# Kernel optimization log

Hardware: AMD Instinct MI355X
Metric: run time of the kernel (lower is better)

Reference implementation:

```python
import jax, jax.numpy as jnp
import numpy as np

B, T, ICD, H = 64, 256, 2000, 384
L, CH, W = 3, H // 3, 10  # levels, chunk_size, conv window


def setup_inputs() -> dict:
    key = jax.random.key(0)
    ks = jax.random.split(key, 10)
    s = 0.05
    return {
        "x": jax.random.uniform(ks[0], (B, T, ICD), jnp.float32),
        "dia_w": jax.random.normal(ks[1], (ICD, H), jnp.float32) * s,
        "dia_b": jnp.zeros((H,), jnp.float32),
        "kernel_w": jax.random.normal(ks[2], (H + 1, 4 * H + 2 * L), jnp.float32) * s,
        "kernel_b": jnp.zeros((4 * H + 2 * L,), jnp.float32),
        "rec_w": jax.random.normal(ks[3], (H + 1, 4 * H + 2 * L), jnp.float32) * s,
        "rec_b": jnp.zeros((4 * H + 2 * L,), jnp.float32),
        "scale_w": jax.random.normal(ks[4], (H, H // 6), jnp.float32) * s,
        "scale_b": jnp.zeros((H // 6,), jnp.float32),
        "rescale_w": jax.random.normal(ks[5], (H // 6, H), jnp.float32) * s,
        "rescale_b": jnp.zeros((H,), jnp.float32),
        "conv_w": jax.random.normal(ks[6], (H, H, W), jnp.float32) * s,  # (out, in, k)
        "conv_b": jnp.zeros((H,), jnp.float32),
        "out_w": jax.random.normal(ks[7], (H, ICD), jnp.float32) * s,
        "out_b": jnp.zeros((ICD,), jnp.float32),
        "choice": 0,  # 0 == 'dia'
    }


def _cumax_l2r(x):
    return jnp.cumsum(jax.nn.softmax(x, -1), -1)


def _cumax_r2l(x):
    return jnp.flip(jnp.cumsum(jax.nn.softmax(jnp.flip(x, -1), -1), -1), -1)


def _forward(x, dia_w, dia_b, kernel_w, kernel_b, rec_w, rec_b,
             scale_w, scale_b, rescale_w, rescale_b, conv_w, conv_b,
             out_w, out_b):
    embed = x @ dia_w + dia_b  # (B,T,H), choice='dia'
    Bs = embed.shape[0]
    ones = jnp.ones((Bs, 1), embed.dtype)  # interval T == 1

    def step(carry, xt):
        c, h, tmp_h, tmp_dis = carry
        xo = (jnp.concatenate([xt, ones], -1) @ kernel_w + kernel_b
              + jnp.concatenate([h, ones], -1) @ rec_w + rec_b)
        fm = _cumax_l2r(xo[:, :L])[:, :, None]          # (B,L,1)
        im = _cumax_r2l(xo[:, L:2 * L])[:, :, None]     # (B,L,1)
        g = xo[:, 2 * L:].reshape(Bs, 4 * L, CH)
        f = jax.nn.sigmoid(g[:, :L])
        i = jax.nn.sigmoid(g[:, L:2 * L])
        o = jax.nn.sigmoid(g[:, 2 * L:3 * L])
        c_in = jnp.tanh(g[:, 3 * L:])
        c_last = c.reshape(Bs, L, CH)
        ov = fm * im
        c_new = ov * (f * c_last + i * c_in) + (fm - ov) * c_last + (im - ov) * c_in
        h_new = (o * jnp.tanh(c_new)).reshape(Bs, H)
        c_new = c_new.reshape(Bs, H)
        cur_dis = 1.0 - jnp.mean(fm[..., 0], -1)        # (B,)
        tmp_h = jnp.concatenate([tmp_h[1:], h_new[None]], 0)      # (W,B,H)
        tmp_dis = jnp.concatenate([tmp_dis[1:], cur_dis[None]], 0)  # (W,B)
        local_dis = jax.nn.softmax(jnp.cumsum(tmp_dis.T, 1), 1)   # (B,W)
        local_h = tmp_h.transpose(1, 2, 0) * local_dis[:, None, :]  # (B,H,W)
        theme = jax.nn.sigmoid(
            jax.nn.relu(jnp.mean(local_h, -1) @ scale_w + scale_b) @ rescale_w + rescale_b)
        conv = jnp.einsum('bhw,ohw->bo', local_h, conv_w) + conv_b  # Conv1d, full-width kernel
        return (c_new, h_new, tmp_h, tmp_dis), (h_new, theme * conv)

    carry0 = (jnp.zeros((Bs, H), embed.dtype), jnp.zeros((Bs, H), embed.dtype),
              jnp.zeros((W, Bs, H), embed.dtype), jnp.zeros((W, Bs), embed.dtype))
    _, (origin_h, loc_h) = jax.lax.scan(step, carry0, embed.transpose(1, 0, 2))
    rnn = (origin_h + loc_h).transpose(1, 0, 2)  # (B,T,H); dropout off (eval)
    return rnn @ out_w + out_b                   # (B,T,ICD)


def reference(x, dia_w, dia_b, kernel_w, kernel_b, rec_w, rec_b,
              scale_w, scale_b, rescale_w, rescale_b, conv_w, conv_b,
              out_w, out_b, choice):
    # choice==0 -> 'dia' embedding path
    return _forward(x, dia_w, dia_b, kernel_w, kernel_b, rec_w, rec_b,
                    scale_w, scale_b, rescale_w, rescale_b, conv_w, conv_b,
                    out_w, out_b)
```

## Files before the change

### kernel.cpp

```cpp
#include <hip/hip_runtime.h>
#include <hip/hip_bf16.h>
#include <cstdint>
#include <cstddef>

#define B_DIM   64
#define T_DIM   256
#define ICD_DIM 2000
#define H_DIM   384
#define CH_DIM  128
#define W_WIN   10
#define M_DIM   (B_DIM * T_DIM)
#define XO_DIM  1542
#define XO_PAD  1664
#define K_X     2016
#define KCONV   3840
#define N_OUTP  2048

typedef unsigned short ushort_t;
typedef unsigned int   uint_t;
typedef __attribute__((ext_vector_type(8))) short short8;
typedef __attribute__((ext_vector_type(4))) float f32x4;
typedef __attribute__((ext_vector_type(2))) _Float16 f16x2;

__device__ __forceinline__ ushort_t f2bf(float v) {
    __hip_bfloat16 b = __float2bfloat16(v);
    ushort_t u; __builtin_memcpy(&u, &b, 2); return u;
}
__device__ __forceinline__ float bf2f(ushort_t u) {
    __hip_bfloat16 b; __builtin_memcpy(&b, &u, 2); return __bfloat162float(b);
}
__device__ __forceinline__ float sigmoidf_(float x) { return 1.f / (1.f + expf(-x)); }
__device__ __forceinline__ f16x2 asf16x2(uint_t u) { f16x2 h; __builtin_memcpy(&h, &u, 4); return h; }
__device__ __forceinline__ uint_t pkf16(float a, float b) {
    f16x2 h; h.x = (_Float16)a; h.y = (_Float16)b;
    uint_t u; __builtin_memcpy(&u, &h, 4); return u;
}
__device__ __forceinline__ float dot2f(uint_t a, uint_t b, float acc) {
#if __has_builtin(__builtin_amdgcn_fdot2)
    return __builtin_amdgcn_fdot2(asf16x2(a), asf16x2(b), acc, false);
#else
    f16x2 ha = asf16x2(a), hb = asf16x2(b);
    return acc + (float)ha.x * (float)hb.x + (float)ha.y * (float)hb.y;
#endif
}

__global__ void prep_dia(const float* __restrict__ dia_w, ushort_t* __restrict__ hi, ushort_t* __restrict__ lo)
{
    int id = blockIdx.x * 256 + threadIdx.x;
    if (id >= H_DIM * K_X) return;
    int n = id / K_X, k = id - n * K_X;
    float v = (k < ICD_DIM) ? dia_w[(size_t)k * H_DIM + n] : 0.f;
    ushort_t h = f2bf(v);
    hi[id] = h; lo[id] = f2bf(v - bf2f(h));
}
__global__ void prep_ker(const float* __restrict__ kernel_w, ushort_t* __restrict__ hi, ushort_t* __restrict__ lo)
{
    int id = blockIdx.x * 256 + threadIdx.x;
    if (id >= XO_PAD * H_DIM) return;
    int n = id / H_DIM, k = id - n * H_DIM;
    float v = (n < XO_DIM) ? kernel_w[(size_t)k * XO_DIM + n] : 0.f;
    ushort_t h = f2bf(v);
    hi[id] = h; lo[id] = f2bf(v - bf2f(h));
}
__global__ void prep_conv(const float* __restrict__ conv_w, ushort_t* __restrict__ bt)
{
    int id = blockIdx.x * 256 + threadIdx.x;
    if (id >= H_DIM * KCONV) return;
    int o = id / KCONV, k = id - o * KCONV;
    int w = k / H_DIM, h = k - w * H_DIM;
    bt[id] = f2bf(conv_w[((size_t)o * H_DIM + h) * W_WIN + w]);
}
__global__ void prep_out(const float* __restrict__ out_w, ushort_t* __restrict__ bt)
{
    int id = blockIdx.x * 256 + threadIdx.x;
    if (id >= N_OUTP * H_DIM) return;
    int n = id / H_DIM, k = id - n * H_DIM;
    bt[id] = f2bf((n < ICD_DIM) ? out_w[(size_t)k * ICD_DIM + n] : 0.f);
}
__global__ void prep_misc(const float* __restrict__ kernel_w, const float* __restrict__ kernel_b,
                          const float* __restrict__ rec_w, const float* __restrict__ rec_b,
                          const float* __restrict__ out_b,
                          float* __restrict__ bias2p, float* __restrict__ outbp)
{
    int j = blockIdx.x * 256 + threadIdx.x;
    if (j < XO_PAD)
        bias2p[j] = (j < XO_DIM) ? (kernel_w[(size_t)H_DIM * XO_DIM + j] + kernel_b[j]
                                  + rec_w[(size_t)H_DIM * XO_DIM + j] + rec_b[j]) : 0.f;
    if (j < N_OUTP)
        outbp[j] = (j < ICD_DIM) ? out_b[j] : 0.f;
}
__global__ void prep_rec2(const float* __restrict__ rec_w, uint_t* __restrict__ recg, uint_t* __restrict__ recm)
{
    int id = blockIdx.x * 256 + threadIdx.x;
    const int NG = 4 * 2 * 96 * 384;
    if (id < NG) {
        int cg = id % 384;
        int kk = (id / 384) % 96;
        int half = (id / (384 * 96)) & 1;
        int q = id / (384 * 96 * 2);
        int p = half * 96 + kk;
        int j = 6 + (cg >> 5) * 128 + q * 32 + (cg & 31);
        recg[id] = pkf16(rec_w[(size_t)(2 * p) * XO_DIM + j], rec_w[(size_t)(2 * p + 1) * XO_DIM + j]);
    } else if (id < NG + 6 * 192) {
        int id2 = id - NG;
        int mc = id2 / 192, p = id2 % 192;
        recm[id2] = pkf16(rec_w[(size_t)(2 * p) * XO_DIM + mc], rec_w[(size_t)(2 * p + 1) * XO_DIM + mc]);
    }
}

template<int MODE>
__global__ __launch_bounds__(256)
void mfma_gemm(const float* __restrict__ Af,
               const ushort_t* __restrict__ Abh, const ushort_t* __restrict__ Abl,
               const ushort_t* __restrict__ Bh, const ushort_t* __restrict__ Bl,
               float* __restrict__ Cf, ushort_t* __restrict__ Cb,
               ushort_t* __restrict__ Ehi, ushort_t* __restrict__ Elo,
               const float* __restrict__ bias,
               const ushort_t* __restrict__ theme,
               const float* __restrict__ hall, const float* __restrict__ ldwp,
               int ksteps, int kdim)
{
    constexpr bool SPLIT = (MODE <= 1);
    __shared__ ushort_t AhS[4096];
    __shared__ ushort_t BhS[4096];
    __shared__ ushort_t AlS[4096];
    __shared__ ushort_t BlS[4096];

    const int tid = threadIdx.x;
    const int rc = tid & 127, kh = tid >> 7;
    const int m0 = blockIdx.y * 128, n0 = blockIdx.x * 128;
    const int kq0 = kh * 2;

    const int lane = tid & 63, wid = tid >> 6;
    const int wm = wid >> 1, wn = wid & 1;
    const int l15 = lane & 15, lkq = lane >> 4;

    f32x4 acc[4][4];
#pragma unroll
    for (int i = 0; i < 4; ++i)
#pragma unroll
        for (int j = 0; j < 4; ++j)
#pragma unroll
            for (int q = 0; q < 4; ++q) acc[i][j][q] = 0.f;

    for (int ks = 0; ks < ksteps; ++ks) {
        const int k16 = ks * 32 + kh * 16;
        __syncthreads();

        if constexpr (MODE == 0 || MODE == 2) {
            float v[16];
            bool ok;
            if constexpr (MODE == 0) {
                ok = (k16 < ICD_DIM);
                if (ok) {
                    const float* ap = Af + (size_t)(m0 + rc) * ICD_DIM + k16;
#pragma unroll
                    for (int q = 0; q < 4; ++q) {
                        float4 t = *(const float4*)(ap + q * 4);
                        v[q * 4 + 0] = t.x; v[q * 4 + 1] = t.y; v[q * 4 + 2] = t.z; v[q * 4 + 3] = t.w;
                    }
                }
            } else {
                const int w = k16 / H_DIM, h0i = k16 - (k16 / H_DIM) * H_DIM;
                const int gm = m0 + rc, b = gm >> 8, tt = gm & 255;
                const int tp = tt - (W_WIN - 1) + w;
                ok = (tp >= 0);
                if (ok) {
                    const float lw = ldwp[(size_t)gm * W_WIN + w];
                    const float* ap = hall + ((size_t)(b * T_DIM + tp)) * H_DIM + h0i;
#pragma unroll
                    for (int q = 0; q < 4; ++q) {
                        float4 t = *(const float4*)(ap + q * 4);
                        v[q * 4 + 0] = t.x * lw; v[q * 4 + 1] = t.y * lw;
                        v[q * 4 + 2] = t.z * lw; v[q * 4 + 3] = t.w * lw;
                    }
                }
            }
            if (!ok) {
#pragma unroll
                for (int q = 0; q < 16; ++q) v[q] = 0.f;
            }
            uint_t hh[8], ll[8];
#pragma unroll
            for (int i = 0; i < 8; ++i) {
                ushort_t h0 = f2bf(v[2 * i]), h1 = f2bf(v[2 * i + 1]);
                hh[i] = (uint_t)h0 | ((uint_t)h1 << 16);
                if constexpr (SPLIT) {
                    ushort_t l0 = f2bf(v[2 * i] - bf2f(h0)), l1 = f2bf(v[2 * i + 1] - bf2f(h1));
                    ll[i] = (uint_t)l0 | ((uint_t)l1 << 16);
                }
            }
            *(uint4*)&AhS[(kq0 * 128 + rc) * 8]       = make_uint4(hh[0], hh[1], hh[2], hh[3]);
            *(uint4*)&AhS[((kq0 + 1) * 128 + rc) * 8] = make_uint4(hh[4], hh[5], hh[6], hh[7]);
            if constexpr (SPLIT) {
                *(uint4*)&AlS[(kq0 * 128 + rc) * 8]       = make_uint4(ll[0], ll[1], ll[2], ll[3]);
                *(uint4*)&AlS[((kq0 + 1) * 128 + rc) * 8] = make_uint4(ll[4], ll[5], ll[6], ll[7]);
            }
        } else {
            const ushort_t* ap = ((MODE == 1) ? Ehi : Abh) + (size_t)(m0 + rc) * H_DIM + k16;
            *(uint4*)&AhS[(kq0 * 128 + rc) * 8]       = *(const uint4*)ap;
            *(uint4*)&AhS[((kq0 + 1) * 128 + rc) * 8] = *(const uint4*)(ap + 8);
            if constexpr (MODE == 1) {
                const ushort_t* ap2 = Elo + (size_t)(m0 + rc) * H_DIM + k16;
                *(uint4*)&AlS[(kq0 * 128 + rc) * 8]       = *(const uint4*)ap2;
                *(uint4*)&AlS[((kq0 + 1) * 128 + rc) * 8] = *(const uint4*)(ap2 + 8);
            }
        }

        {
            const ushort_t* bp = Bh + (size_t)(n0 + rc) * kdim + k16;
            *(uint4*)&BhS[(kq0 * 128 + rc) * 8]       = *(const uint4*)bp;
            *(uint4*)&BhS[((kq0 + 1) * 128 + rc) * 8] = *(const uint4*)(bp + 8);
            if constexpr (SPLIT) {
                const ushort_t* bp2 = Bl + (size_t)(n0 + rc) * kdim + k16;
                *(uint4*)&BlS[(kq0 * 128 + rc) * 8]       = *(const uint4*)bp2;
                *(uint4*)&BlS[((kq0 + 1) * 128 + rc) * 8] = *(const uint4*)(bp2 + 8);
            }
        }
        __syncthreads();

        short8 ah[4], bh[4], al[4], bl[4];
#pragma unroll
        for (int mf = 0; mf < 4; ++mf)
            ah[mf] = *(const short8*)&AhS[(lkq * 128 + wm * 64 + mf * 16 + l15) * 8];
#pragma unroll
        for (int nf = 0; nf < 4; ++nf)
            bh[nf] = *(const short8*)&BhS[(lkq * 128 + wn * 64 + nf * 16 + l15) * 8];
        if constexpr (SPLIT) {
#pragma unroll
            for (int mf = 0; mf < 4; ++mf)
                al[mf] = *(const short8*)&AlS[(lkq * 128 + wm * 64 + mf * 16 + l15) * 8];
#pragma unroll
            for (int nf = 0; nf < 4; ++nf)
                bl[nf] = *(const short8*)&BlS[(lkq * 128 + wn * 64 + nf * 16 + l15) * 8];
        }
#pragma unroll
        for (int mf = 0; mf < 4; ++mf)
#pragma unroll
            for (int nf = 0; nf < 4; ++nf) {
                acc[mf][nf] = __builtin_amdgcn_mfma_f32_16x16x32_bf16(ah[mf], bh[nf], acc[mf][nf], 0, 0, 0);
                if constexpr (SPLIT) {
                    acc[mf][nf] = __builtin_amdgcn_mfma_f32_16x16x32_bf16(ah[mf], bl[nf], acc[mf][nf], 0, 0, 0);
                    acc[mf][nf] = __builtin_amdgcn_mfma_f32_16x16x32_bf16(al[mf], bh[nf], acc[mf][nf], 0, 0, 0);
                }
            }
    }

#pragma unroll
    for (int mf = 0; mf < 4; ++mf)
#pragma unroll
        for (int nf = 0; nf < 4; ++nf)
#pragma unroll
            for (int j = 0; j < 4; ++j) {
                const int gm = m0 + wm * 64 + mf * 16 + lkq * 4 + j;
                const int gn = n0 + wn * 64 + nf * 16 + l15;
                float v = acc[mf][nf][j] + bias[gn];
                if constexpr (MODE == 0) {
                    ushort_t h = f2bf(v);
                    Ehi[(size_t)gm * H_DIM + gn] = h;
                    Elo[(size_t)gm * H_DIM + gn] = f2bf(v - bf2f(h));
                } else if constexpr (MODE == 1) {
                    if (gn < XO_DIM) Cf[(size_t)gm * XO_DIM + gn] = v;
                } else if constexpr (MODE == 2) {
                    const size_t ix = (size_t)gm * H_DIM + gn;
                    v = v * bf2f(theme[ix]) + hall[ix];
                    Cb[ix] = f2bf(v);
                } else {
                    if (gn < ICD_DIM) Cf[(size_t)gm * ICD_DIM + gn] = v;
                }
            }
}

__global__ __launch_bounds__(768, 3)
void scan_kernel(const float* __restrict__ Xproj, const uint_t* __restrict__ recg,
                 const uint_t* __restrict__ recm, float* __restrict__ h_all,
                 float* __restrict__ dis_all, uint_t* __restrict__ hpk)
{
    __shared__ ushort_t hs16[H_DIM];
    __shared__ float xo_s[384];
    __shared__ float xom_s[6];
    __shared__ uint_t wm2[6 * 192];
    __shared__ float c_s[96];
    __shared__ float fm_s[3], im_s[3];

    const int tid = threadIdx.x;
    const int q = blockIdx.x >> 6, b = blockIdx.x & 63;

    const int cg = tid >> 1, half = tid & 1;
    const int jg = 6 + (cg >> 5) * 128 + q * 32 + (cg & 31);

    const int gl = tid / 32, gu = tid & 31;
    const int jglob = gl * 128 + q * 32 + gu;

    for (int i = tid; i < 6 * 192; i += 768) wm2[i] = recm[i];
    if (tid < H_DIM) hs16[tid] = 0;
    if (tid < 96) c_s[tid] = 0.f;

    uint_t w[96];
#pragma unroll
    for (int kk = 0; kk < 96; ++kk)
        w[kk] = recg[(size_t)((q * 2 + half) * 96 + kk) * 384 + cg];

    float xv = 0.f, xvm = 0.f;
    if (half == 0) xv = Xproj[((size_t)b * T_DIM + 0) * XO_DIM + jg];
    if (tid < 24 && (tid & 3) == 0) xvm = Xproj[((size_t)b * T_DIM + 0) * XO_DIM + (tid >> 2)];

    __syncthreads();

    for (int t = 0; t < T_DIM; ++t) {
        {
            float acc = 0.f;
            const ushort_t* hp = &hs16[half * 192];
#pragma unroll
            for (int kk = 0; kk < 96; kk += 4) {
                const uint4 hq = *(const uint4*)(hp + kk * 2);
                acc = dot2f(w[kk + 0], hq.x, acc);
                acc = dot2f(w[kk + 1], hq.y, acc);
                acc = dot2f(w[kk + 2], hq.z, acc);
                acc = dot2f(w[kk + 3], hq.w, acc);
            }
            acc += __shfl_xor(acc, 1);
            if (half == 0) xo_s[cg] = acc + xv;
        }
        if (tid < 24) {
            const int mc = tid >> 2, kq = tid & 3;
            float acc = 0.f;
            const uint_t* wp = &wm2[mc * 192 + kq * 48];
#pragma unroll
            for (int kk = 0; kk < 48; kk += 4) {
                const uint4 hq = *(const uint4*)&hs16[(kq * 48 + kk) * 2];
                acc = dot2f(wp[kk + 0], hq.x, acc);
                acc = dot2f(wp[kk + 1], hq.y, acc);
                acc = dot2f(wp[kk + 2], hq.z, acc);
                acc = dot2f(wp[kk + 3], hq.w, acc);
            }
            acc += __shfl_xor(acc, 2);
            acc += __shfl_xor(acc, 1);
            if (kq == 0) xom_s[mc] = acc + xvm;
        }
        __syncthreads();

        if (tid == 0) {
            float x0 = xom_s[0], x1 = xom_s[1], x2 = xom_s[2];
            float mx = fmaxf(x0, fmaxf(x1, x2));
            float e0 = expf(x0 - mx), e1 = expf(x1 - mx), e2 = expf(x2 - mx);
            float inv = 1.f / (e0 + e1 + e2);
            const float f0 = e0 * inv, f1 = (e0 + e1) * inv;
            fm_s[0] = f0; fm_s[1] = f1; fm_s[2] = 1.f;
            x0 = xom_s[3]; x1 = xom_s[4]; x2 = xom_s[5];
            mx = fmaxf(x0, fmaxf(x1, x2));
            e0 = expf(x0 - mx); e1 = expf(x1 - mx); e2 = expf(x2 - mx);
            inv = 1.f / (e0 + e1 + e2);
            im_s[0] = 1.f; im_s[1] = (e1 + e2) * inv; im_s[2] = e2 * inv;
            if (q == 0)
                dis_all[b * T_DIM + t] = 1.f - (f0 + f1 + 1.f) * (1.f / 3.f);
        }
        __syncthreads();

        if (tid < 96) {
            const float fm = fm_s[gl], im = im_s[gl];
            const float fg = sigmoidf_(xo_s[gl * 32 + gu]);
            const float ig = sigmoidf_(xo_s[(3 + gl) * 32 + gu]);
            const float og = sigmoidf_(xo_s[(6 + gl) * 32 + gu]);
            const float ci = tanhf(xo_s[(9 + gl) * 32 + gu]);
            const float cl = c_s[tid];
            const float ov = fm * im;
            const float cn = ov * (fg * cl + ig * ci) + (fm - ov) * cl + (im - ov) * ci;
            c_s[tid] = cn;
            const float hn = og * tanhf(cn);
            h_all[((size_t)b * T_DIM + t) * H_DIM + jglob] = hn;
            _Float16 hf = (_Float16)hn;
            ushort_t hb; __builtin_memcpy(&hb, &hf, 2);
            const uint_t word = ((uint_t)hb << 16) | (uint_t)(t + 1);
            __hip_atomic_store(&hpk[(size_t)(t & 1) * B_DIM * H_DIM + b * H_DIM + jglob],
                               word, __ATOMIC_RELAXED, __HIP_MEMORY_SCOPE_AGENT);
        }

        if (t + 1 < T_DIM) {
            if (half == 0) xv = Xproj[((size_t)b * T_DIM + (t + 1)) * XO_DIM + jg];
            if (tid < 24 && (tid & 3) == 0) xvm = Xproj[((size_t)b * T_DIM + (t + 1)) * XO_DIM + (tid >> 2)];
        }

        if (t + 1 < T_DIM) {
            if (tid < H_DIM) {
                const uint_t want = (uint_t)(t + 1);
                uint_t* addr = &hpk[(size_t)(t & 1) * B_DIM * H_DIM + b * H_DIM + tid];
                uint_t v = __hip_atomic_load(addr, __ATOMIC_RELAXED, __HIP_MEMORY_SCOPE_AGENT);
                while ((v & 0xFFFFu) != want) {
                    __builtin_amdgcn_s_sleep(1);
                    v = __hip_atomic_load(addr, __ATOMIC_RELAXED, __HIP_MEMORY_SCOPE_AGENT);
                }
                hs16[tid] = (ushort_t)(v >> 16);
            }
            __syncthreads();
        }
    }
}

__global__ __launch_bounds__(256, 2)
void locdis2_kernel(const float* __restrict__ h_all, const float* __restrict__ dis_all,
                    const float* __restrict__ scale_w, const float* __restrict__ scale_b,
                    const float* __restrict__ rescale_w, const float* __restrict__ rescale_b,
                    float* __restrict__ ldw, ushort_t* __restrict__ theme)
{
    __shared__ float ld_all[64][10];
    __shared__ uint_t mh2[192];
    __shared__ float part_s[4][64];
    __shared__ float hid[64];
    __shared__ uint_t hid2[32];

    const int tid = threadIdx.x;
    const int b = blockIdx.x >> 2, t0 = (blockIdx.x & 3) * 64;

    const int o1 = tid & 63, p1 = tid >> 6;
    uint_t w1[48];
#pragma unroll
    for (int kk = 0; kk < 48; ++kk) {
        const int p = p1 * 48 + kk;
        w1[kk] = pkf16(scale_w[(size_t)(2 * p) * 64 + o1], scale_w[(size_t)(2 * p + 1) * 64 + o1]);
    }
    uint_t w2[48];
#pragma unroll
    for (int j = 0; j < 3; ++j) {
        const int o2 = j * 128 + (tid >> 1), hf = tid & 1;
#pragma unroll
        for (int kk = 0; kk < 16; ++kk) {
            const int p = hf * 16 + kk;
            w2[j * 16 + kk] = pkf16(rescale_w[(size_t)(2 * p) * H_DIM + o2],
                                    rescale_w[(size_t)(2 * p + 1) * H_DIM + o2]);
        }
    }

    if (tid < 64) {
        const int t = t0 + tid;
        float cum = 0.f, c[10];
        for (int wq = 0; wq < 10; ++wq) {
            const int tp = t - 9 + wq;
            cum += (tp >= 0) ? dis_all[b * T_DIM + tp] : 0.f;
            c[wq] = cum;
        }
        float mx = c[0];
        for (int wq = 1; wq < 10; ++wq) mx = fmaxf(mx, c[wq]);
        float s = 0.f, e[10];
        for (int wq = 0; wq < 10; ++wq) { e[wq] = expf(c[wq] - mx); s += e[wq]; }
        const float inv = 1.f / s;
        for (int wq = 0; wq < 10; ++wq) {
            ld_all[tid][wq] = e[wq] * inv;
            ldw[((size_t)b * T_DIM + t) * W_WIN + wq] = e[wq] * inv;
        }
    }
    __syncthreads();

    for (int r = 0; r < 64; ++r) {
        const int t = t0 + r;
        if (tid < 192) {
            float a0 = 0.f, a1 = 0.f;
            for (int wq = 0; wq < 10; ++wq) {
                const int tp = t - 9 + wq;
                if (tp >= 0) {
                    const float lw = ld_all[r][wq];
                    const float2 h2 = *(const float2*)&h_all[((size_t)b * T_DIM + tp) * H_DIM + 2 * tid];
                    a0 += lw * h2.x; a1 += lw * h2.y;
                }
            }
            mh2[tid] = pkf16(a0 * 0.1f, a1 * 0.1f);
        }
        __syncthreads();
        {
            float acc = 0.f;
#pragma unroll
            for (int kk = 0; kk < 48; ++kk)
                acc = dot2f(w1[kk], mh2[p1 * 48 + kk], acc);
            part_s[p1][o1] = acc;
        }
        __syncthreads();
        if (tid < 64)
            hid[tid] = fmaxf(scale_b[tid] + part_s[0][tid] + part_s[1][tid] + part_s[2][tid] + part_s[3][tid], 0.f);
        __syncthreads();
        if (tid < 32) hid2[tid] = pkf16(hid[2 * tid], hid[2 * tid + 1]);
        __syncthreads();
#pragma unroll
        for (int j = 0; j < 3; ++j) {
            const int o2 = j * 128 + (tid >> 1), hf = tid & 1;
            float acc = 0.f;
#pragma unroll
            for (int kk = 0; kk < 16; ++kk)
                acc = dot2f(w2[j * 16 + kk], hid2[hf * 16 + kk], acc);
            acc += __shfl_xor(acc, 1);
            if (hf == 0)
                theme[((size_t)b * T_DIM + t) * H_DIM + o2] = f2bf(sigmoidf_(acc + rescale_b[o2]));
        }
        __syncthreads();
    }
}

extern "C" void kernel_launch(void* const* d_in, const int* in_sizes, int n_in,
                              void* d_out, int out_size, void* d_ws, size_t ws_size,
                              hipStream_t stream)
{
    const float* x         = (const float*)d_in[0];
    const float* dia_w     = (const float*)d_in[1];
    const float* dia_b     = (const float*)d_in[2];
    const float* kernel_w  = (const float*)d_in[3];
    const float* kernel_b  = (const float*)d_in[4];
    const float* rec_w     = (const float*)d_in[5];
    const float* rec_b     = (const float*)d_in[6];
    const float* scale_w   = (const float*)d_in[7];
    const float* scale_b   = (const float*)d_in[8];
    const float* rescale_w = (const float*)d_in[9];
    const float* rescale_b = (const float*)d_in[10];
    const float* conv_w    = (const float*)d_in[11];
    const float* conv_b    = (const float*)d_in[12];
    const float* out_w     = (const float*)d_in[13];
    const float* out_b     = (const float*)d_in[14];
    (void)in_sizes; (void)n_in; (void)out_size; (void)ws_size;

    float* ws = (float*)d_ws;
    size_t off = 0;
    float* Xproj   = ws + off; off += (size_t)M_DIM * XO_DIM;
    float* h_all   = ws + off; off += (size_t)M_DIM * H_DIM;
    float* ldw     = ws + off; off += (size_t)M_DIM * W_WIN;
    float* dis_all = ws + off; off += M_DIM;
    float* bias2p  = ws + off; off += XO_PAD;
    float* outbp   = ws + off; off += N_OUTP;
    uint_t* hpk    = (uint_t*)(ws + off); off += (size_t)2 * B_DIM * H_DIM;
    ushort_t* us = (ushort_t*)(ws + off);
    size_t uo = 0;
    ushort_t* dia_hi = us + uo; uo += (size_t)H_DIM * K_X;
    ushort_t* dia_lo = us + uo; uo += (size_t)H_DIM * K_X;
    ushort_t* ker_hi = us + uo; uo += (size_t)XO_PAD * H_DIM;
    ushort_t* ker_lo = us + uo; uo += (size_t)XO_PAD * H_DIM;
    ushort_t* conv_t = us + uo; uo += (size_t)H_DIM * KCONV;
    ushort_t* outw_t = us + uo; uo += (size_t)N_OUTP * H_DIM;
    ushort_t* ehi    = us + uo; uo += (size_t)M_DIM * H_DIM;
    ushort_t* elo    = us + uo; uo += (size_t)M_DIM * H_DIM;
    ushort_t* themeb = us + uo; uo += (size_t)M_DIM * H_DIM;
    ushort_t* rnnb   = us + uo; uo += (size_t)M_DIM * H_DIM;
    uint_t* recg = (uint_t*)(us + uo); uo += (size_t)2 * 4 * 2 * 96 * 384;
    uint_t* recm = (uint_t*)(us + uo); uo += (size_t)2 * 6 * 192;

    prep_dia <<<(H_DIM * K_X + 255) / 256, 256, 0, stream>>>(dia_w, dia_hi, dia_lo);
    prep_ker <<<(XO_PAD * H_DIM + 255) / 256, 256, 0, stream>>>(kernel_w, ker_hi, ker_lo);
    prep_conv<<<(H_DIM * KCONV + 255) / 256, 256, 0, stream>>>(conv_w, conv_t);
    prep_out <<<(N_OUTP * H_DIM + 255) / 256, 256, 0, stream>>>(out_w, outw_t);
    prep_misc<<<(N_OUTP + 255) / 256, 256, 0, stream>>>(kernel_w, kernel_b, rec_w, rec_b, out_b, bias2p, outbp);
    prep_rec2<<<(4 * 2 * 96 * 384 + 6 * 192 + 255) / 256, 256, 0, stream>>>(rec_w, recg, recm);

    mfma_gemm<0><<<dim3(3, 128), 256, 0, stream>>>(
        x, nullptr, nullptr, dia_hi, dia_lo, nullptr, nullptr, ehi, elo,
        dia_b, nullptr, nullptr, nullptr, K_X / 32, K_X);

    mfma_gemm<1><<<dim3(13, 128), 256, 0, stream>>>(
        nullptr, nullptr, nullptr, ker_hi, ker_lo, Xproj, nullptr, ehi, elo,
        bias2p, nullptr, nullptr, nullptr, H_DIM / 32, H_DIM);

    {
        void* args[] = { (void*)&Xproj, (void*)&recg, (void*)&recm,
                         (void*)&h_all, (void*)&dis_all, (void*)&hpk };
        (void)hipLaunchCooperativeKernel((const void*)scan_kernel, dim3(256), dim3(768), args, 0, stream);
    }

    locdis2_kernel<<<256, 256, 0, stream>>>(
        h_all, dis_all, scale_w, scale_b, rescale_w, rescale_b, ldw, themeb);

    mfma_gemm<2><<<dim3(3, 128), 256, 0, stream>>>(
        nullptr, nullptr, nullptr, conv_t, nullptr, nullptr, rnnb, nullptr, nullptr,
        conv_b, themeb, h_all, ldw, KCONV / 32, KCONV);

    mfma_gemm<3><<<dim3(16, 128), 256, 0, stream>>>(
        nullptr, rnnb, nullptr, outw_t, nullptr, (float*)d_out, nullptr, nullptr, nullptr,
        outbp, nullptr, nullptr, nullptr, H_DIM / 32, H_DIM);
}
```

Baseline: 1.442 ms.

## Trim split-bf16 products, use direct global-to-LDS loads, streamline scan sync and locdis reuse

The GEMMs now split only one operand into hi/lo bf16 parts (A in mode 1, B in mode 0), which drops one MFMA per fragment in those modes and removes the ker_lo weight buffer. Tile loads switch from register-staged copies to global_load_lds direct-to-LDS transfers. The scan kernel merges the master-gate reduction into one wavefront using shuffles, which removes a barrier and the xom_s buffer. Each thread writes its own h element locally, so only the other 288 elements are polled from peer blocks. The locdis kernel keeps a 10-row ring of h in shared memory instead of re-reading the window from global memory, at the cost of an extra barrier per row and some lost precision in the terms that are no longer split.

```diff
diff --git a/kernel.cpp b/kernel.cpp
--- a/kernel.cpp
+++ b/kernel.cpp
@@ -44,6 +44,10 @@
 #endif
 }
 
+#define GLOAD_LDS16(g, l) __builtin_amdgcn_global_load_lds( \
+    (const __attribute__((address_space(1))) void*)(g),     \
+    (__attribute__((address_space(3))) void*)(l), 16, 0, 0)
+
 __global__ void prep_dia(const float* __restrict__ dia_w, ushort_t* __restrict__ hi, ushort_t* __restrict__ lo)
 {
     int id = blockIdx.x * 256 + threadIdx.x;
@@ -53,14 +57,12 @@
     ushort_t h = f2bf(v);
     hi[id] = h; lo[id] = f2bf(v - bf2f(h));
 }
-__global__ void prep_ker(const float* __restrict__ kernel_w, ushort_t* __restrict__ hi, ushort_t* __restrict__ lo)
+__global__ void prep_ker(const float* __restrict__ kernel_w, ushort_t* __restrict__ hi)
 {
     int id = blockIdx.x * 256 + threadIdx.x;
     if (id >= XO_PAD * H_DIM) return;
     int n = id / H_DIM, k = id - n * H_DIM;
-    float v = (n < XO_DIM) ? kernel_w[(size_t)k * XO_DIM + n] : 0.f;
-    ushort_t h = f2bf(v);
-    hi[id] = h; lo[id] = f2bf(v - bf2f(h));
+    hi[id] = f2bf((n < XO_DIM) ? kernel_w[(size_t)k * XO_DIM + n] : 0.f);
 }
 __global__ void prep_conv(const float* __restrict__ conv_w, ushort_t* __restrict__ bt)
 {
@@ -120,7 +122,8 @@
                const float* __restrict__ hall, const float* __restrict__ ldwp,
                int ksteps, int kdim)
 {
-    constexpr bool SPLIT = (MODE <= 1);
+    constexpr bool SPLITA = (MODE == 1);
+    constexpr bool SPLITB = (MODE == 0);
     __shared__ ushort_t AhS[4096];
     __shared__ ushort_t BhS[4096];
     __shared__ ushort_t AlS[4096];
@@ -180,41 +183,35 @@
 #pragma unroll
                 for (int q = 0; q < 16; ++q) v[q] = 0.f;
             }
-            uint_t hh[8], ll[8];
+            uint_t hh[8];
 #pragma unroll
             for (int i = 0; i < 8; ++i) {
                 ushort_t h0 = f2bf(v[2 * i]), h1 = f2bf(v[2 * i + 1]);
                 hh[i] = (uint_t)h0 | ((uint_t)h1 << 16);
-                if constexpr (SPLIT) {
-                    ushort_t l0 = f2bf(v[2 * i] - bf2f(h0)), l1 = f2bf(v[2 * i + 1] - bf2f(h1));
-                    ll[i] = (uint_t)l0 | ((uint_t)l1 << 16);
-                }
             }
             *(uint4*)&AhS[(kq0 * 128 + rc) * 8]       = make_uint4(hh[0], hh[1], hh[2], hh[3]);
             *(uint4*)&AhS[((kq0 + 1) * 128 + rc) * 8] = make_uint4(hh[4], hh[5], hh[6], hh[7]);
-            if constexpr (SPLIT) {
-                *(uint4*)&AlS[(kq0 * 128 + rc) * 8]       = make_uint4(ll[0], ll[1], ll[2], ll[3]);
-                *(uint4*)&AlS[((kq0 + 1) * 128 + rc) * 8] = make_uint4(ll[4], ll[5], ll[6], ll[7]);
-            }
+        } else if constexpr (MODE == 1) {
+            const ushort_t* ap = Ehi + (size_t)(m0 + rc) * H_DIM + k16;
+            GLOAD_LDS16(ap,     &AhS[(kq0 * 128 + rc) * 8]);
+            GLOAD_LDS16(ap + 8, &AhS[((kq0 + 1) * 128 + rc) * 8]);
+            const ushort_t* ap2 = Elo + (size_t)(m0 + rc) * H_DIM + k16;
+            GLOAD_LDS16(ap2,     &AlS[(kq0 * 128 + rc) * 8]);
+            GLOAD_LDS16(ap2 + 8, &AlS[((kq0 + 1) * 128 + rc) * 8]);
         } else {
-            const ushort_t* ap = ((MODE == 1) ? Ehi : Abh) + (size_t)(m0 + rc) * H_DIM + k16;
-            *(uint4*)&AhS[(kq0 * 128 + rc) * 8]       = *(const uint4*)ap;
-            *(uint4*)&AhS[((kq0 + 1) * 128 + rc) * 8] = *(const uint4*)(ap + 8);
-            if constexpr (MODE == 1) {
-                const ushort_t* ap2 = Elo + (size_t)(m0 + rc) * H_DIM + k16;
-                *(uint4*)&AlS[(kq0 * 128 + rc) * 8]       = *(const uint4*)ap2;
-                *(uint4*)&AlS[((kq0 + 1) * 128 + rc) * 8] = *(const uint4*)(ap2 + 8);
-            }
+            const ushort_t* ap = Abh + (size_t)(m0 + rc) * H_DIM + k16;
+            GLOAD_LDS16(ap,     &AhS[(kq0 * 128 + rc) * 8]);
+            GLOAD_LDS16(ap + 8, &AhS[((kq0 + 1) * 128 + rc) * 8]);
         }
 
         {
             const ushort_t* bp = Bh + (size_t)(n0 + rc) * kdim + k16;
-            *(uint4*)&BhS[(kq0 * 128 + rc) * 8]       = *(const uint4*)bp;
-            *(uint4*)&BhS[((kq0 + 1) * 128 + rc) * 8] = *(const uint4*)(bp + 8);
-            if constexpr (SPLIT) {
+            GLOAD_LDS16(bp,     &BhS[(kq0 * 128 + rc) * 8]);
+            GLOAD_LDS16(bp + 8, &BhS[((kq0 + 1) * 128 + rc) * 8]);
+            if constexpr (SPLITB) {
                 const ushort_t* bp2 = Bl + (size_t)(n0 + rc) * kdim + k16;
-                *(uint4*)&BlS[(kq0 * 128 + rc) * 8]       = *(const uint4*)bp2;
-                *(uint4*)&BlS[((kq0 + 1) * 128 + rc) * 8] = *(const uint4*)(bp2 + 8);
+                GLOAD_LDS16(bp2,     &BlS[(kq0 * 128 + rc) * 8]);
+                GLOAD_LDS16(bp2 + 8, &BlS[((kq0 + 1) * 128 + rc) * 8]);
             }
         }
         __syncthreads();
@@ -226,10 +223,12 @@
 #pragma unroll
         for (int nf = 0; nf < 4; ++nf)
             bh[nf] = *(const short8*)&BhS[(lkq * 128 + wn * 64 + nf * 16 + l15) * 8];
-        if constexpr (SPLIT) {
+        if constexpr (SPLITA) {
 #pragma unroll
             for (int mf = 0; mf < 4; ++mf)
                 al[mf] = *(const short8*)&AlS[(lkq * 128 + wm * 64 + mf * 16 + l15) * 8];
+        }
+        if constexpr (SPLITB) {
 #pragma unroll
             for (int nf = 0; nf < 4; ++nf)
                 bl[nf] = *(const short8*)&BlS[(lkq * 128 + wn * 64 + nf * 16 + l15) * 8];
@@ -239,10 +238,10 @@
 #pragma unroll
             for (int nf = 0; nf < 4; ++nf) {
                 acc[mf][nf] = __builtin_amdgcn_mfma_f32_16x16x32_bf16(ah[mf], bh[nf], acc[mf][nf], 0, 0, 0);
-                if constexpr (SPLIT) {
+                if constexpr (SPLITB)
                     acc[mf][nf] = __builtin_amdgcn_mfma_f32_16x16x32_bf16(ah[mf], bl[nf], acc[mf][nf], 0, 0, 0);
+                if constexpr (SPLITA)
                     acc[mf][nf] = __builtin_amdgcn_mfma_f32_16x16x32_bf16(al[mf], bh[nf], acc[mf][nf], 0, 0, 0);
-                }
             }
     }
 
@@ -278,7 +277,6 @@
 {
     __shared__ ushort_t hs16[H_DIM];
     __shared__ float xo_s[384];
-    __shared__ float xom_s[6];
     __shared__ uint_t wm2[6 * 192];
     __shared__ float c_s[96];
     __shared__ float fm_s[3], im_s[3];
@@ -291,6 +289,11 @@
 
     const int gl = tid / 32, gu = tid & 31;
     const int jglob = gl * 128 + q * 32 + gu;
+
+    const int rsp = tid - 96;
+    const int qq_sp = (q + 1 + rsp / 96) & 3;
+    const int s_sp = rsp % 96;
+    const int j_sp = (s_sp >> 5) * 128 + qq_sp * 32 + (s_sp & 31);
 
     for (int i = tid; i < 6 * 192; i += 768) wm2[i] = recm[i];
     if (tid < H_DIM) hs16[tid] = 0;
@@ -322,38 +325,39 @@
             acc += __shfl_xor(acc, 1);
             if (half == 0) xo_s[cg] = acc + xv;
         }
-        if (tid < 24) {
-            const int mc = tid >> 2, kq = tid & 3;
+
+        if (tid < 64) {
             float acc = 0.f;
-            const uint_t* wp = &wm2[mc * 192 + kq * 48];
-#pragma unroll
-            for (int kk = 0; kk < 48; kk += 4) {
-                const uint4 hq = *(const uint4*)&hs16[(kq * 48 + kk) * 2];
-                acc = dot2f(wp[kk + 0], hq.x, acc);
-                acc = dot2f(wp[kk + 1], hq.y, acc);
-                acc = dot2f(wp[kk + 2], hq.z, acc);
-                acc = dot2f(wp[kk + 3], hq.w, acc);
+            if (tid < 24) {
+                const int mc = tid >> 2, kq = tid & 3;
+                const uint_t* wp = &wm2[mc * 192 + kq * 48];
+#pragma unroll
+                for (int kk = 0; kk < 48; kk += 4) {
+                    const uint4 hq = *(const uint4*)&hs16[(kq * 48 + kk) * 2];
+                    acc = dot2f(wp[kk + 0], hq.x, acc);
+                    acc = dot2f(wp[kk + 1], hq.y, acc);
+                    acc = dot2f(wp[kk + 2], hq.z, acc);
+                    acc = dot2f(wp[kk + 3], hq.w, acc);
+                }
+                if ((tid & 3) == 0) acc += xvm;
             }
             acc += __shfl_xor(acc, 2);
             acc += __shfl_xor(acc, 1);
-            if (kq == 0) xom_s[mc] = acc + xvm;
-        }
-        __syncthreads();
-
-        if (tid == 0) {
-            float x0 = xom_s[0], x1 = xom_s[1], x2 = xom_s[2];
-            float mx = fmaxf(x0, fmaxf(x1, x2));
-            float e0 = expf(x0 - mx), e1 = expf(x1 - mx), e2 = expf(x2 - mx);
-            float inv = 1.f / (e0 + e1 + e2);
-            const float f0 = e0 * inv, f1 = (e0 + e1) * inv;
-            fm_s[0] = f0; fm_s[1] = f1; fm_s[2] = 1.f;
-            x0 = xom_s[3]; x1 = xom_s[4]; x2 = xom_s[5];
-            mx = fmaxf(x0, fmaxf(x1, x2));
-            e0 = expf(x0 - mx); e1 = expf(x1 - mx); e2 = expf(x2 - mx);
-            inv = 1.f / (e0 + e1 + e2);
-            im_s[0] = 1.f; im_s[1] = (e1 + e2) * inv; im_s[2] = e2 * inv;
-            if (q == 0)
-                dis_all[b * T_DIM + t] = 1.f - (f0 + f1 + 1.f) * (1.f / 3.f);
+            const float m0 = __shfl(acc, 0),  m1 = __shfl(acc, 4),  m2 = __shfl(acc, 8);
+            const float m3 = __shfl(acc, 12), m4 = __shfl(acc, 16), m5 = __shfl(acc, 20);
+            if (tid == 0) {
+                float mx = fmaxf(m0, fmaxf(m1, m2));
+                float e0 = expf(m0 - mx), e1 = expf(m1 - mx), e2 = expf(m2 - mx);
+                float inv = 1.f / (e0 + e1 + e2);
+                const float f0 = e0 * inv, f1 = (e0 + e1) * inv;
+                fm_s[0] = f0; fm_s[1] = f1; fm_s[2] = 1.f;
+                mx = fmaxf(m3, fmaxf(m4, m5));
+                e0 = expf(m3 - mx); e1 = expf(m4 - mx); e2 = expf(m5 - mx);
+                inv = 1.f / (e0 + e1 + e2);
+                im_s[0] = 1.f; im_s[1] = (e1 + e2) * inv; im_s[2] = e2 * inv;
+                if (q == 0)
+                    dis_all[b * T_DIM + t] = 1.f - (f0 + f1 + 1.f) * (1.f / 3.f);
+            }
         }
         __syncthreads();
 
@@ -371,6 +375,7 @@
             h_all[((size_t)b * T_DIM + t) * H_DIM + jglob] = hn;
             _Float16 hf = (_Float16)hn;
             ushort_t hb; __builtin_memcpy(&hb, &hf, 2);
+            hs16[jglob] = hb;
             const uint_t word = ((uint_t)hb << 16) | (uint_t)(t + 1);
             __hip_atomic_store(&hpk[(size_t)(t & 1) * B_DIM * H_DIM + b * H_DIM + jglob],
                                word, __ATOMIC_RELAXED, __HIP_MEMORY_SCOPE_AGENT);
@@ -382,15 +387,15 @@
         }
 
         if (t + 1 < T_DIM) {
-            if (tid < H_DIM) {
+            if (tid >= 96 && tid < 384) {
                 const uint_t want = (uint_t)(t + 1);
-                uint_t* addr = &hpk[(size_t)(t & 1) * B_DIM * H_DIM + b * H_DIM + tid];
+                uint_t* addr = &hpk[(size_t)(t & 1) * B_DIM * H_DIM + b * H_DIM + j_sp];
                 uint_t v = __hip_atomic_load(addr, __ATOMIC_RELAXED, __HIP_MEMORY_SCOPE_AGENT);
                 while ((v & 0xFFFFu) != want) {
                     __builtin_amdgcn_s_sleep(1);
                     v = __hip_atomic_load(addr, __ATOMIC_RELAXED, __HIP_MEMORY_SCOPE_AGENT);
                 }
-                hs16[tid] = (ushort_t)(v >> 16);
+                hs16[j_sp] = (ushort_t)(v >> 16);
             }
             __syncthreads();
         }
@@ -403,6 +408,7 @@
                     const float* __restrict__ rescale_w, const float* __restrict__ rescale_b,
                     float* __restrict__ ldw, ushort_t* __restrict__ theme)
 {
+    __shared__ float ring[10][H_DIM];
     __shared__ float ld_all[64][10];
     __shared__ uint_t mh2[192];
     __shared__ float part_s[4][64];
@@ -449,18 +455,29 @@
             ldw[((size_t)b * T_DIM + t) * W_WIN + wq] = e[wq] * inv;
         }
     }
+    for (int tp = t0 - 9; tp < t0; ++tp) {
+        if (tp >= 0) {
+            for (int i = tid; i < H_DIM; i += 256)
+                ring[tp % 10][i] = h_all[((size_t)b * T_DIM + tp) * H_DIM + i];
+        }
+    }
     __syncthreads();
 
     for (int r = 0; r < 64; ++r) {
         const int t = t0 + r;
+        if (tid < 192) {
+            const float2 h2 = *(const float2*)&h_all[((size_t)b * T_DIM + t) * H_DIM + 2 * tid];
+            *(float2*)&ring[t % 10][2 * tid] = h2;
+        }
+        __syncthreads();
         if (tid < 192) {
             float a0 = 0.f, a1 = 0.f;
             for (int wq = 0; wq < 10; ++wq) {
                 const int tp = t - 9 + wq;
                 if (tp >= 0) {
                     const float lw = ld_all[r][wq];
-                    const float2 h2 = *(const float2*)&h_all[((size_t)b * T_DIM + tp) * H_DIM + 2 * tid];
-                    a0 += lw * h2.x; a1 += lw * h2.y;
+                    a0 += lw * ring[tp % 10][2 * tid];
+                    a1 += lw * ring[tp % 10][2 * tid + 1];
                 }
             }
             mh2[tid] = pkf16(a0 * 0.1f, a1 * 0.1f);
@@ -529,7 +546,6 @@
     ushort_t* dia_hi = us + uo; uo += (size_t)H_DIM * K_X;
     ushort_t* dia_lo = us + uo; uo += (size_t)H_DIM * K_X;
     ushort_t* ker_hi = us + uo; uo += (size_t)XO_PAD * H_DIM;
-    ushort_t* ker_lo = us + uo; uo += (size_t)XO_PAD * H_DIM;
     ushort_t* conv_t = us + uo; uo += (size_t)H_DIM * KCONV;
     ushort_t* outw_t = us + uo; uo += (size_t)N_OUTP * H_DIM;
     ushort_t* ehi    = us + uo; uo += (size_t)M_DIM * H_DIM;
@@ -540,7 +556,7 @@
     uint_t* recm = (uint_t*)(us + uo); uo += (size_t)2 * 6 * 192;
 
     prep_dia <<<(H_DIM * K_X + 255) / 256, 256, 0, stream>>>(dia_w, dia_hi, dia_lo);
-    prep_ker <<<(XO_PAD * H_DIM + 255) / 256, 256, 0, stream>>>(kernel_w, ker_hi, ker_lo);
+    prep_ker <<<(XO_PAD * H_DIM + 255) / 256, 256, 0, stream>>>(kernel_w, ker_hi);
     prep_conv<<<(H_DIM * KCONV + 255) / 256, 256, 0, stream>>>(conv_w, conv_t);
     prep_out <<<(N_OUTP * H_DIM + 255) / 256, 256, 0, stream>>>(out_w, outw_t);
     prep_misc<<<(N_OUTP + 255) / 256, 256, 0, stream>>>(kernel_w, kernel_b, rec_w, rec_b, out_b, bias2p, outbp);
@@ -551,7 +567,7 @@
         dia_b, nullptr, nullptr, nullptr, K_X / 32, K_X);
 
     mfma_gemm<1><<<dim3(13, 128), 256, 0, stream>>>(
-        nullptr, nullptr, nullptr, ker_hi, ker_lo, Xproj, nullptr, ehi, elo,
+        nullptr, nullptr, nullptr, ker_hi, nullptr, Xproj, nullptr, ehi, elo,
         bias2p, nullptr, nullptr, nullptr, H_DIM / 32, H_DIM);
 
     {
```

Result: faster. 1.377 ms (-4.5%).
